# Kernel tuning notes

Hardware: AMD Instinct MI355X
Metric: run time of the kernel (lower is better)

Reference implementation:

```python
import jax, jax.numpy as jnp
import numpy as np

DIM = 384
DH = 32
H = DIM // DH          # 12 heads
N_WIN = 3072           # total windows
W_ACT = 1536           # active windows = M
T = 64                 # tokens per window (8x8)
NTOK = W_ACT * T       # 98304 active tokens
N_BLOCK = 9830
MLP = 4 * DIM
EPS = 1e-5


def _layer_norm(h, w, b):
    mu = jnp.mean(h, axis=-1, keepdims=True)
    var = jnp.mean(jnp.square(h - mu), axis=-1, keepdims=True)
    return (h - mu) * jax.lax.rsqrt(var + EPS) * w + b


def setup_inputs() -> dict:
    key = jax.random.key(0)
    ks = jax.random.split(key, 16)
    x = jax.random.normal(ks[0], (N_WIN, T, DIM), jnp.float32)
    # unique active windows, sorted (scatter-restore requires uniqueness)
    index_window = jnp.sort(jax.random.permutation(ks[1], N_WIN)[:W_ACT])
    # full permutation of active tokens into M groups of size S
    index_partition = jax.random.permutation(ks[2], NTOK)
    blocked_index = jax.random.permutation(ks[3], NTOK)[:N_BLOCK]
    s = 0.02
    params = dict(
        ln1_w=jnp.ones((DIM,), jnp.float32), ln1_b=jnp.zeros((DIM,), jnp.float32),
        qkv_w=jax.random.normal(ks[4], (3 * DIM, DIM), jnp.float32) * s,
        qkv_b=jnp.zeros((3 * DIM,), jnp.float32),
        proj_w=jax.random.normal(ks[5], (DIM, DIM), jnp.float32) * s,
        proj_b=jnp.zeros((DIM,), jnp.float32),
        ln2_w=jnp.ones((DIM,), jnp.float32), ln2_b=jnp.zeros((DIM,), jnp.float32),
        fc1_w=jax.random.normal(ks[6], (MLP, DIM), jnp.float32) * s,
        fc1_b=jnp.zeros((MLP,), jnp.float32),
        fc2_w=jax.random.normal(ks[7], (DIM, MLP), jnp.float32) * s,
        fc2_b=jnp.zeros((DIM,), jnp.float32),
    )
    return dict(x=x, index_window=index_window, index_partition=index_partition,
                blocked_index=blocked_index, M=W_ACT, K=jnp.zeros((1,), jnp.int64),
                **params)


def reference(x, index_window, index_partition, blocked_index, M, K,
              ln1_w, ln1_b, qkv_w, qkv_b, proj_w, proj_b,
              ln2_w, ln2_b, fc1_w, fc1_b, fc2_w, fc2_b):
    N, T_, C = x.shape
    scale = DH ** -0.5
    S = index_partition.shape[0] // M

    xn = _layer_norm(x, ln1_w, ln1_b)                      # (N, T, C)
    xw = xn[index_window].reshape(-1, C)                   # (NTOK, C) active tokens
    xp = xw[index_partition].reshape(M, S, C)              # (M, S, C) regrouped
    shortcut = xp

    qkv = (xp @ qkv_w.T + qkv_b).reshape(M, S, H, 3 * DH)  # per-head [q|k|v] chunks
    q, k, v = qkv[..., :DH], qkv[..., DH:2 * DH], qkv[..., 2 * DH:]

    attn = jnp.einsum('mqhd,mkhd->mhqk', q, k) * scale     # (M, H, Sq, Sk)

    # scatter scores into full-size map keyed by KEY token, mask blocked keys, gather back
    amap = jnp.zeros((xw.shape[0], S, H), attn.dtype)      # (NTOK, Sq, H)
    amap = amap.at[index_partition].set(jnp.transpose(attn, (0, 3, 2, 1)).reshape(-1, S, H))
    amap = amap.at[blocked_index].set(-10000.0)
    attn = jnp.transpose(amap[index_partition].reshape(M, S, S, H), (0, 3, 2, 1))
    attn = jax.nn.softmax(attn, axis=-1)

    o = jnp.einsum('mhqk,mkhd->mqhd', attn, v).reshape(M, S, C)
    o = o @ proj_w.T + proj_b

    # sub_layers: [Id, Id(+res), LN, fc1, GELU, fc2(+res)]
    h = shortcut + o
    shortcut = h
    h2 = _layer_norm(h, ln2_w, ln2_b)
    h2 = jax.nn.gelu(h2 @ fc1_w.T + fc1_b, approximate=False)
    h = shortcut + (h2 @ fc2_w.T + fc2_b)

    # scatter-restore: blocked tokens keep their (normed) input values
    XX = xw.at[index_partition].set(h.reshape(-1, C))
    XX = XX.at[blocked_index].set(xw[blocked_index])
    out = xn.at[index_window].set(XX.reshape(M, -1, C))
    return out
```

## Files before the change

### kernel.cpp

```cpp
#include <hip/hip_runtime.h>
#include <hip/hip_bf16.h>

typedef __attribute__((ext_vector_type(8))) short bf16x8;
typedef __attribute__((ext_vector_type(4))) short s16x4;
typedef __attribute__((ext_vector_type(4))) float f32x4;
typedef __attribute__((ext_vector_type(2))) long longx2;
typedef __attribute__((ext_vector_type(16))) unsigned char u8x16;

#define NW_   3072
#define WACT_ 1536
#define NTOK_ 98304
#define NBLK_ 9830
#define DIM_  384
#define QKVD_ 1152
#define MLPD_ 1536

__device__ __forceinline__ float bf2f(short s) {
  union { unsigned u; float f; } c;
  c.u = ((unsigned)(unsigned short)s) << 16;
  return c.f;
}
__device__ __forceinline__ short f2bf(float f) {
  union { float f; unsigned u; } c; c.f = f;
  unsigned lsb = (c.u >> 16) & 1u;
  c.u += 0x7fffu + lsb;
  return (short)(c.u >> 16);
}

__device__ __forceinline__ f32x4 mfma8(long a, long b, f32x4 c) {
  return __builtin_amdgcn_mfma_f32_16x16x32_fp8_fp8(a, b, c, 0, 0, 0);
}

__device__ __forceinline__ void gload16(const void* g, void* l) {
  __builtin_amdgcn_global_load_lds(
      (const __attribute__((address_space(1))) unsigned*)g,
      (__attribute__((address_space(3))) unsigned*)l, 16, 0, 0);
}

__device__ __forceinline__ int kperm(int col) {
  int l = (col >> 3) & 7;
  int s = ((l & 3) << 1) | (l >> 2);
  return (col & ~63) + s * 8 + (col & 7);
}

__device__ __forceinline__ void conv8_chunk(const float* __restrict__ src,
                                            unsigned char* __restrict__ dst,
                                            int K, int blk, int tid) {
  int i = (blk * 256 + tid) * 8;
  f32x4 v0 = *(const f32x4*)&src[i];
  f32x4 v1 = *(const f32x4*)&src[i + 4];
  int w0 = __builtin_amdgcn_cvt_pk_fp8_f32(v0[0], v0[1], 0, false);
  w0 = __builtin_amdgcn_cvt_pk_fp8_f32(v0[2], v0[3], w0, true);
  int w1 = __builtin_amdgcn_cvt_pk_fp8_f32(v1[0], v1[1], 0, false);
  w1 = __builtin_amdgcn_cvt_pk_fp8_f32(v1[2], v1[3], w1, true);
  int kro = i % K, row = i / K;
  union { int u[2]; long ll; } p; p.u[0] = w0; p.u[1] = w1;
  *(long*)&dst[(size_t)row * K + kperm(kro)] = p.ll;
}

__global__ __launch_bounds__(256) void pre_k(const float* __restrict__ qkvw,
                                             const float* __restrict__ projw,
                                             const float* __restrict__ fc1w,
                                             const float* __restrict__ fc2w,
                                             unsigned char* __restrict__ qw8,
                                             unsigned char* __restrict__ pw8,
                                             unsigned char* __restrict__ f1w8,
                                             unsigned char* __restrict__ f2w8,
                                             int* win_rank, unsigned* bitmap) {
  const int bid = blockIdx.x, tid = threadIdx.x;
  if (bid < 12) {
    int t = bid * 256 + tid;
    if (t < NW_) { win_rank[t] = -1; bitmap[t] = 0u; }
  } else if (bid < 228) {
    conv8_chunk(qkvw, qw8, 384, bid - 12, tid);
  } else if (bid < 300) {
    conv8_chunk(projw, pw8, 384, bid - 228, tid);
  } else if (bid < 588) {
    conv8_chunk(fc1w, f1w8, 384, bid - 300, tid);
  } else {
    conv8_chunk(fc2w, f2w8, MLPD_, bid - 588, tid);
  }
}

__global__ __launch_bounds__(256) void mapB_k(const int* __restrict__ iw,
                                              const int* __restrict__ blk,
                                              int* win_rank, unsigned* bitmap) {
  int t = blockIdx.x * 256 + threadIdx.x;
  if (t < WACT_) win_rank[iw[t]] = t;
  if (t < NBLK_) { int j = blk[t]; atomicOr(&bitmap[j >> 5], 1u << (j & 31)); }
}

__global__ __launch_bounds__(256) void mapC_k(const int* __restrict__ ip,
                                              const int* __restrict__ iw,
                                              const unsigned* __restrict__ bitmap,
                                              int* inv_ip, int* rowmap) {
  int i = blockIdx.x * 256 + threadIdx.x;
  if (i < NTOK_) {
    int j = ip[i];
    inv_ip[j] = i;
    int blocked = (bitmap[j >> 5] >> (j & 31)) & 1;
    rowmap[i] = blocked ? -1 : (iw[j >> 6] * 64 + (j & 63));
  }
}

__global__ __launch_bounds__(256) void ln1_k(const float* __restrict__ x,
                                             const float* __restrict__ w,
                                             const float* __restrict__ b,
                                             const int* __restrict__ win_rank,
                                             const int* __restrict__ inv_ip,
                                             const unsigned* __restrict__ bitmap,
                                             float* __restrict__ out,
                                             short* __restrict__ xp,
                                             unsigned char* __restrict__ xp8) {
  const int l = threadIdx.x & 31;
  const int tok = blockIdx.x * 8 + (threadIdx.x >> 5);
  const f32x4* xr = (const f32x4*)(x + (size_t)tok * DIM_);
  f32x4 v[3]; float s = 0.f;
#pragma unroll
  for (int j = 0; j < 3; ++j) {
    v[j] = xr[l + 32 * j];
    s += v[j][0] + v[j][1] + v[j][2] + v[j][3];
  }
#pragma unroll
  for (int m = 1; m <= 16; m <<= 1) s += __shfl_xor(s, m, 64);
  float mu = s * (1.0f / DIM_);
  float q = 0.f;
#pragma unroll
  for (int j = 0; j < 3; ++j)
#pragma unroll
    for (int e = 0; e < 4; ++e) { float d = v[j][e] - mu; q += d * d; }
#pragma unroll
  for (int m = 1; m <= 16; m <<= 1) q += __shfl_xor(q, m, 64);
  float rs = rsqrtf(q * (1.0f / DIM_) + 1e-5f);
  f32x4 y[3];
#pragma unroll
  for (int j = 0; j < 3; ++j) {
    f32x4 wv = *(const f32x4*)&w[4 * l + 128 * j];
    f32x4 bv = *(const f32x4*)&b[4 * l + 128 * j];
#pragma unroll
    for (int e = 0; e < 4; ++e) y[j][e] = (v[j][e] - mu) * rs * wv[e] + bv[e];
  }
  int wdw = tok >> 6, t = tok & 63;
  int rank = win_rank[wdw];
  if (rank < 0) {
    f32x4* po = (f32x4*)(out + (size_t)tok * DIM_);
#pragma unroll
    for (int j = 0; j < 3; ++j) po[l + 32 * j] = y[j];
  } else {
    int jdx = (rank << 6) + t;
    int i = inv_ip[jdx];
#pragma unroll
    for (int j = 0; j < 3; ++j) {
      s16x4 o;
#pragma unroll
      for (int e = 0; e < 4; ++e) o[e] = f2bf(y[j][e]);
      *(s16x4*)&xp[(size_t)i * DIM_ + 4 * l + 128 * j] = o;
      int wrd = __builtin_amdgcn_cvt_pk_fp8_f32(y[j][0], y[j][1], 0, false);
      wrd = __builtin_amdgcn_cvt_pk_fp8_f32(y[j][2], y[j][3], wrd, true);
      *(unsigned*)&xp8[(size_t)i * DIM_ + kperm(4 * l + 128 * j)] = (unsigned)wrd;
    }
    if ((bitmap[jdx >> 5] >> (jdx & 31)) & 1) {
      f32x4* po = (f32x4*)(out + (size_t)tok * DIM_);
#pragma unroll
      for (int j = 0; j < 3; ++j) po[l + 32 * j] = y[j];
    }
  }
}

__global__ __launch_bounds__(256) void ln2_k(const short* __restrict__ h,
                                             const float* __restrict__ w,
                                             const float* __restrict__ b,
                                             unsigned char* __restrict__ out8) {
  const int l = threadIdx.x & 31;
  const int tok = blockIdx.x * 8 + (threadIdx.x >> 5);
  const s16x4* xr = (const s16x4*)(h + (size_t)tok * DIM_);
  float v[12]; float s = 0.f;
#pragma unroll
  for (int j = 0; j < 3; ++j) {
    s16x4 rv = xr[l + 32 * j];
#pragma unroll
    for (int e = 0; e < 4; ++e) { v[j * 4 + e] = bf2f(rv[e]); s += v[j * 4 + e]; }
  }
#pragma unroll
  for (int m = 1; m <= 16; m <<= 1) s += __shfl_xor(s, m, 64);
  float mu = s * (1.0f / DIM_);
  float q = 0.f;
#pragma unroll
  for (int e = 0; e < 12; ++e) { float d = v[e] - mu; q += d * d; }
#pragma unroll
  for (int m = 1; m <= 16; m <<= 1) q += __shfl_xor(q, m, 64);
  float rs = rsqrtf(q * (1.0f / DIM_) + 1e-5f);
#pragma unroll
  for (int j = 0; j < 3; ++j) {
    f32x4 wv = *(const f32x4*)&w[4 * l + 128 * j];
    f32x4 bv = *(const f32x4*)&b[4 * l + 128 * j];
    float y[4];
#pragma unroll
    for (int e = 0; e < 4; ++e)
      y[e] = (v[j * 4 + e] - mu) * rs * wv[e] + bv[e];
    int wrd = __builtin_amdgcn_cvt_pk_fp8_f32(y[0], y[1], 0, false);
    wrd = __builtin_amdgcn_cvt_pk_fp8_f32(y[2], y[3], wrd, true);
    int c0 = 4 * l + 128 * j;
    *(unsigned*)&out8[(size_t)tok * DIM_ + kperm(c0)] = (unsigned)wrd;
  }
}

template <int EPI>
__global__ __launch_bounds__(512) void gemmf8_k(const unsigned char* __restrict__ A8,
                                                const unsigned char* __restrict__ B8,
                                                const float* __restrict__ bias,
                                                int K, int nx,
                                                short* __restrict__ Cb,
                                                unsigned char* __restrict__ C8,
                                                const short* __restrict__ add_bf,
                                                const int* __restrict__ rowmap,
                                                float* __restrict__ outf) {
  const int nwg = gridDim.x;
  const int q8 = nwg >> 3;
  const int wg = (blockIdx.x & 7) * q8 + (blockIdx.x >> 3);
  const int ntile = wg % nx, mtile = wg / nx;
  const int tid = threadIdx.x, wid = tid >> 6, lane = tid & 63;
  const int fq = lane >> 4, fr = lane & 15;
  const int wr = wid >> 1, wc = wid & 1;
  __shared__ __align__(16) unsigned char lA[256 * 128];
  __shared__ __align__(16) unsigned char lB[128 * 128];
  const int row0 = mtile * 256, col0 = ntile * 128;
  float bs[4];
#pragma unroll
  for (int nt = 0; nt < 4; ++nt) bs[nt] = bias[col0 + wc * 64 + nt * 16 + fr];
  f32x4 acc[4][4];
#pragma unroll
  for (int a = 0; a < 4; ++a)
#pragma unroll
    for (int c = 0; c < 4; ++c) acc[a][c] = (f32x4){0.f, 0.f, 0.f, 0.f};
  const int nkt = K >> 7;
  for (int kt = 0; kt < nkt; ++kt) {
    const int k0 = kt << 7;
#pragma unroll
    for (int i = 0; i < 4; ++i) {
      int g = i * 512 + tid;
      int r = g >> 3, c8 = g & 7;
      int s8 = c8 ^ (r & 7);
      gload16(A8 + (size_t)(row0 + r) * K + k0 + s8 * 16, (char*)lA + (size_t)g * 16);
    }
#pragma unroll
    for (int i = 0; i < 2; ++i) {
      int g = i * 512 + tid;
      int r = g >> 3, c8 = g & 7;
      int s8 = c8 ^ (r & 7);
      gload16(B8 + (size_t)(col0 + r) * K + k0 + s8 * 16, (char*)lB + (size_t)g * 16);
    }
    __syncthreads();
#pragma unroll
    for (int ss = 0; ss < 2; ++ss) {
      longx2 af[4], bfr[4];
      const int pb = ss * 4 + fq;
#pragma unroll
      for (int mt = 0; mt < 4; ++mt) {
        int r = wr * 64 + mt * 16 + fr;
        int d = pb ^ (r & 7);
        af[mt] = *(const longx2*)&lA[r * 128 + d * 16];
      }
#pragma unroll
      for (int nt = 0; nt < 4; ++nt) {
        int r = wc * 64 + nt * 16 + fr;
        int d = pb ^ (r & 7);
        bfr[nt] = *(const longx2*)&lB[r * 128 + d * 16];
      }
#pragma unroll
      for (int mt = 0; mt < 4; ++mt)
#pragma unroll
        for (int nt = 0; nt < 4; ++nt) {
          acc[mt][nt] = mfma8(af[mt][0], bfr[nt][0], acc[mt][nt]);
          acc[mt][nt] = mfma8(af[mt][1], bfr[nt][1], acc[mt][nt]);
        }
    }
    __syncthreads();
  }
#pragma unroll
  for (int mt = 0; mt < 4; ++mt) {
#pragma unroll
    for (int jj = 0; jj < 4; ++jj) {
      int r = row0 + wr * 64 + mt * 16 + fq * 4 + jj;
      int dmap = 0;
      if (EPI == 3) dmap = rowmap[r];
      if (EPI == 0) {
        float g4[4];
#pragma unroll
        for (int nt = 0; nt < 4; ++nt) g4[nt] = acc[mt][nt][jj] + bs[nt];
        int p01 = __builtin_amdgcn_cvt_pk_fp8_f32(g4[0], g4[1], 0, false);
        int p23 = __builtin_amdgcn_cvt_pk_fp8_f32(g4[2], g4[3], 0, false);
        const size_t rb = (size_t)r * QKVD_ + col0 + wc * 64 + fr;
        C8[rb]      = (unsigned char)(p01 & 0xff);
        C8[rb + 16] = (unsigned char)((p01 >> 8) & 0xff);
        C8[rb + 32] = (unsigned char)(p23 & 0xff);
        C8[rb + 48] = (unsigned char)((p23 >> 8) & 0xff);
      } else if (EPI == 1) {
#pragma unroll
        for (int nt = 0; nt < 4; ++nt) {
          int gcol = col0 + wc * 64 + nt * 16 + fr;
          float v = acc[mt][nt][jj] + bs[nt] + bf2f(add_bf[(size_t)r * DIM_ + gcol]);
          Cb[(size_t)r * DIM_ + gcol] = f2bf(v);
        }
      } else if (EPI == 2) {
        float g4[4];
#pragma unroll
        for (int nt = 0; nt < 4; ++nt) {
          float v = acc[mt][nt][jj] + bs[nt];
          float u = v * (0.79788456f + 0.03567741f * v * v);
          g4[nt] = v * __builtin_amdgcn_rcpf(1.0f + __expf(-2.0f * u));
        }
        int p01 = __builtin_amdgcn_cvt_pk_fp8_f32(g4[0], g4[1], 0, false);
        int p23 = __builtin_amdgcn_cvt_pk_fp8_f32(g4[2], g4[3], 0, false);
        const int C0 = col0 + wc * 64;
        const size_t rb = (size_t)r * MLPD_ + C0 + (fr & 7) + ((fr >> 3) << 4);
        C8[rb]      = (unsigned char)(p01 & 0xff);
        C8[rb + 32] = (unsigned char)((p01 >> 8) & 0xff);
        C8[rb + 8]  = (unsigned char)(p23 & 0xff);
        C8[rb + 40] = (unsigned char)((p23 >> 8) & 0xff);
      } else {
#pragma unroll
        for (int nt = 0; nt < 4; ++nt) {
          int gcol = col0 + wc * 64 + nt * 16 + fr;
          float v = acc[mt][nt][jj] + bs[nt] + bf2f(add_bf[(size_t)r * DIM_ + gcol]);
          if (dmap >= 0) outf[(size_t)dmap * DIM_ + gcol] = v;
        }
      }
    }
  }
}

__global__ __launch_bounds__(256) void attn_k(const unsigned char* __restrict__ qkv8,
                                              const unsigned* __restrict__ bitmap,
                                              const int* __restrict__ ip,
                                              unsigned char* __restrict__ o8) {
  const int flat = (blockIdx.x & 7) * 576 + (blockIdx.x >> 3);
  const int m = flat / 3;
  const int h = (flat % 3) * 4 + (threadIdx.x >> 6);
  const int wid = threadIdx.x >> 6, lane = threadIdx.x & 63;
  const int fq = lane >> 4, fr = lane & 15;
  __shared__ __align__(16) unsigned char P[4][64 * 72];
  __shared__ __align__(16) unsigned char Vt[4][32 * 72];
  __shared__ unsigned char flags[64];
  if (threadIdx.x < 64) {
    int j = ip[m * 64 + threadIdx.x];
    flags[threadIdx.x] = (unsigned char)((bitmap[j >> 5] >> (j & 31)) & 1);
  }
  __syncthreads();
  const float scale = 0.17677669529663687f;
  int msk[4];
#pragma unroll
  for (int nt = 0; nt < 4; ++nt) msk[nt] = flags[nt * 16 + fr];

  const unsigned char* base = qkv8 + (size_t)m * 64 * QKVD_ + h * 96;
  f32x4 sacc[4][4];
#pragma unroll
  for (int a = 0; a < 4; ++a)
#pragma unroll
    for (int c = 0; c < 4; ++c) sacc[a][c] = (f32x4){0.f, 0.f, 0.f, 0.f};
  long qa[4], kb[4];
#pragma unroll
  for (int mt = 0; mt < 4; ++mt)
    qa[mt] = *(const long*)(base + (size_t)(mt * 16 + fr) * QKVD_ + fq * 8);
#pragma unroll
  for (int nt = 0; nt < 4; ++nt)
    kb[nt] = *(const long*)(base + (size_t)(nt * 16 + fr) * QKVD_ + 32 + fq * 8);
#pragma unroll
  for (int mt = 0; mt < 4; ++mt)
#pragma unroll
    for (int nt = 0; nt < 4; ++nt)
      sacc[mt][nt] = mfma8(qa[mt], kb[nt], sacc[mt][nt]);
#pragma unroll
  for (int c = 0; c < 2; ++c) {
    u8x16 vv = *(const u8x16*)(base + (size_t)lane * QKVD_ + 64 + c * 16);
#pragma unroll
    for (int e = 0; e < 16; ++e) Vt[wid][(c * 16 + e) * 72 + lane] = vv[e];
  }
#pragma unroll
  for (int mt = 0; mt < 4; ++mt)
#pragma unroll
    for (int nt = 0; nt < 4; ++nt) {
      f32x4 sv = sacc[mt][nt];
#pragma unroll
      for (int jj = 0; jj < 4; ++jj)
        sv[jj] = msk[nt] ? -10000.0f : sv[jj] * scale;
      sacc[mt][nt] = sv;
    }
#pragma unroll
  for (int mt = 0; mt < 4; ++mt) {
#pragma unroll
    for (int jj = 0; jj < 4; ++jj) {
      float mx = sacc[mt][0][jj];
#pragma unroll
      for (int nt = 1; nt < 4; ++nt) mx = fmaxf(mx, sacc[mt][nt][jj]);
#pragma unroll
      for (int mm = 1; mm < 16; mm <<= 1) mx = fmaxf(mx, __shfl_xor(mx, mm, 64));
      float sm = 0.f;
      float p[4];
#pragma unroll
      for (int nt = 0; nt < 4; ++nt) {
        p[nt] = __expf(sacc[mt][nt][jj] - mx);
        sm += p[nt];
      }
#pragma unroll
      for (int mm = 1; mm < 16; mm <<= 1) sm += __shfl_xor(sm, mm, 64);
      float inv = 1.0f / sm;
      int rowb = (mt * 16 + fq * 4 + jj) * 72;
      int p01 = __builtin_amdgcn_cvt_pk_fp8_f32(p[0] * inv, p[1] * inv, 0, false);
      int p23 = __builtin_amdgcn_cvt_pk_fp8_f32(p[2] * inv, p[3] * inv, 0, false);
      P[wid][rowb + fr]      = (unsigned char)(p01 & 0xff);
      P[wid][rowb + 16 + fr] = (unsigned char)((p01 >> 8) & 0xff);
      P[wid][rowb + 32 + fr] = (unsigned char)(p23 & 0xff);
      P[wid][rowb + 48 + fr] = (unsigned char)((p23 >> 8) & 0xff);
    }
  }
  f32x4 oacc[4][2];
#pragma unroll
  for (int a = 0; a < 4; ++a)
#pragma unroll
    for (int c = 0; c < 2; ++c) oacc[a][c] = (f32x4){0.f, 0.f, 0.f, 0.f};
#pragma unroll
  for (int ks = 0; ks < 2; ++ks) {
    long pa[4], vb[2];
#pragma unroll
    for (int mt = 0; mt < 4; ++mt)
      pa[mt] = *(const long*)&P[wid][(mt * 16 + fr) * 72 + ks * 32 + fq * 8];
#pragma unroll
    for (int nd = 0; nd < 2; ++nd)
      vb[nd] = *(const long*)&Vt[wid][(nd * 16 + fr) * 72 + ks * 32 + fq * 8];
#pragma unroll
    for (int mt = 0; mt < 4; ++mt)
#pragma unroll
      for (int nd = 0; nd < 2; ++nd)
        oacc[mt][nd] = mfma8(pa[mt], vb[nd], oacc[mt][nd]);
  }
  const int pos0 = kperm(h * 32 + fr);
  const int pos1 = kperm(h * 32 + 16 + fr);
#pragma unroll
  for (int mt = 0; mt < 4; ++mt)
#pragma unroll
    for (int jj = 0; jj < 4; ++jj) {
      int p01 = __builtin_amdgcn_cvt_pk_fp8_f32(oacc[mt][0][jj], oacc[mt][1][jj],
                                                0, false);
      size_t rb = (size_t)(m * 64 + mt * 16 + fq * 4 + jj) * DIM_;
      o8[rb + pos0] = (unsigned char)(p01 & 0xff);
      o8[rb + pos1] = (unsigned char)((p01 >> 8) & 0xff);
    }
}

extern "C" void kernel_launch(void* const* d_in, const int* in_sizes, int n_in,
                              void* d_out, int out_size, void* d_ws, size_t ws_size,
                              hipStream_t stream) {
  const float* x = (const float*)d_in[0];
  const int* iw = (const int*)d_in[1];
  const int* ip = (const int*)d_in[2];
  const int* blk = (const int*)d_in[3];
  const float* ln1w = (const float*)d_in[6];
  const float* ln1b = (const float*)d_in[7];
  const float* qkvw = (const float*)d_in[8];
  const float* qkvb = (const float*)d_in[9];
  const float* projw = (const float*)d_in[10];
  const float* projb = (const float*)d_in[11];
  const float* ln2w = (const float*)d_in[12];
  const float* ln2b = (const float*)d_in[13];
  const float* fc1w = (const float*)d_in[14];
  const float* fc1b = (const float*)d_in[15];
  const float* fc2w = (const float*)d_in[16];
  const float* fc2b = (const float*)d_in[17];
  float* out = (float*)d_out;

  char* ws = (char*)d_ws;
  unsigned char* qkvw8 = (unsigned char*)ws;
  unsigned char* projw8 = (unsigned char*)(ws + 442368);
  unsigned char* fc1w8 = (unsigned char*)(ws + 589824);
  unsigned char* fc2w8 = (unsigned char*)(ws + 1179648);
  int* inv_ip = (int*)(ws + 2211840);
  int* rowmap = inv_ip + NTOK_;
  int* win_rank = rowmap + NTOK_;
  unsigned* bitmap = (unsigned*)(win_rank + NW_);
  short* xp = (short*)(ws + 4349952);
  unsigned char* qkv8 = (unsigned char*)(ws + 79847424);
  unsigned char* t8 = qkv8;
  unsigned char* obuf8 = (unsigned char*)(ws + 306339840);
  unsigned char* ln2buf8 = (unsigned char*)(ws + 344088576);
  unsigned char* xp8 = (unsigned char*)(ws + 381837312);
  short* hbuf = (short*)(ws + 457334784);
  (void)in_sizes; (void)n_in; (void)out_size; (void)ws_size;

  pre_k<<<876, 256, 0, stream>>>(qkvw, projw, fc1w, fc2w, qkvw8, projw8, fc1w8,
                                 fc2w8, win_rank, bitmap);
  mapB_k<<<39, 256, 0, stream>>>(iw, blk, win_rank, bitmap);
  mapC_k<<<NTOK_ / 256, 256, 0, stream>>>(ip, iw, bitmap, inv_ip, rowmap);
  ln1_k<<<(NW_ * 64) / 8, 256, 0, stream>>>(x, ln1w, ln1b, win_rank, inv_ip, bitmap,
                                            out, xp, xp8);
  gemmf8_k<0><<<384 * 9, 512, 0, stream>>>(xp8, qkvw8, qkvb, 384, 9, nullptr,
                                           qkv8, nullptr, nullptr, nullptr);
  attn_k<<<WACT_ * 3, 256, 0, stream>>>(qkv8, bitmap, ip, obuf8);
  gemmf8_k<1><<<384 * 3, 512, 0, stream>>>(obuf8, projw8, projb, 384, 3, hbuf,
                                           nullptr, xp, nullptr, nullptr);
  ln2_k<<<NTOK_ / 8, 256, 0, stream>>>(hbuf, ln2w, ln2b, ln2buf8);
  gemmf8_k<2><<<384 * 12, 512, 0, stream>>>(ln2buf8, fc1w8, fc1b, 384, 12, nullptr,
                                            t8, nullptr, nullptr, nullptr);
  gemmf8_k<3><<<384 * 3, 512, 0, stream>>>(t8, fc2w8, fc2b, MLPD_, 3, nullptr,
                                           nullptr, hbuf, rowmap, out);
}
```

Baseline: 609.7 us.

## Stage window QKV rows into swizzled LDS with coalesced loads in attention kernel

Measured after the change: 609.4 us (median of 2 runs). No clear change (-0.1%).

```diff
diff --git a/kernel.cpp b/kernel.cpp
--- a/kernel.cpp
+++ b/kernel.cpp
@@ -5,7 +5,6 @@
 typedef __attribute__((ext_vector_type(4))) short s16x4;
 typedef __attribute__((ext_vector_type(4))) float f32x4;
 typedef __attribute__((ext_vector_type(2))) long longx2;
-typedef __attribute__((ext_vector_type(16))) unsigned char u8x16;
 
 #define NW_   3072
 #define WACT_ 1536
@@ -336,23 +335,39 @@
                                               unsigned char* __restrict__ o8) {
   const int flat = (blockIdx.x & 7) * 576 + (blockIdx.x >> 3);
   const int m = flat / 3;
-  const int h = (flat % 3) * 4 + (threadIdx.x >> 6);
+  const int grp = flat % 3;
   const int wid = threadIdx.x >> 6, lane = threadIdx.x & 63;
+  const int h = grp * 4 + wid;
   const int fq = lane >> 4, fr = lane & 15;
-  __shared__ __align__(16) unsigned char P[4][64 * 72];
+  __shared__ __align__(16) unsigned char qkvL[24576];
   __shared__ __align__(16) unsigned char Vt[4][32 * 72];
   __shared__ unsigned char flags[64];
+  unsigned char (*P)[64 * 72] = (unsigned char (*)[64 * 72])qkvL;
+
+  const unsigned char* rowbase = qkv8 + (size_t)m * 64 * QKVD_ + grp * 384;
+#pragma unroll
+  for (int i = 0; i < 6; ++i) {
+    int g = i * 256 + threadIdx.x;
+    int r = g / 24, c16 = g % 24;
+    int sc = c16 ^ (r & 7);
+    gload16(rowbase + (size_t)r * QKVD_ + sc * 16, (char*)qkvL + (size_t)g * 16);
+  }
   if (threadIdx.x < 64) {
     int j = ip[m * 64 + threadIdx.x];
     flags[threadIdx.x] = (unsigned char)((bitmap[j >> 5] >> (j & 31)) & 1);
   }
   __syncthreads();
+
   const float scale = 0.17677669529663687f;
   int msk[4];
 #pragma unroll
   for (int nt = 0; nt < 4; ++nt) msk[nt] = flags[nt * 16 + fr];
 
-  const unsigned char* base = qkv8 + (size_t)m * 64 * QKVD_ + h * 96;
+  auto ldsc = [&](int r, int c) -> long {
+    int slot = (c >> 1) ^ (r & 7);
+    return *(const long*)&qkvL[r * 384 + slot * 16 + (c & 1) * 8];
+  };
+
   f32x4 sacc[4][4];
 #pragma unroll
   for (int a = 0; a < 4; ++a)
@@ -360,22 +375,23 @@
     for (int c = 0; c < 4; ++c) sacc[a][c] = (f32x4){0.f, 0.f, 0.f, 0.f};
   long qa[4], kb[4];
 #pragma unroll
-  for (int mt = 0; mt < 4; ++mt)
-    qa[mt] = *(const long*)(base + (size_t)(mt * 16 + fr) * QKVD_ + fq * 8);
-#pragma unroll
-  for (int nt = 0; nt < 4; ++nt)
-    kb[nt] = *(const long*)(base + (size_t)(nt * 16 + fr) * QKVD_ + 32 + fq * 8);
+  for (int mt = 0; mt < 4; ++mt) qa[mt] = ldsc(mt * 16 + fr, wid * 12 + fq);
+#pragma unroll
+  for (int nt = 0; nt < 4; ++nt) kb[nt] = ldsc(nt * 16 + fr, wid * 12 + 4 + fq);
 #pragma unroll
   for (int mt = 0; mt < 4; ++mt)
 #pragma unroll
     for (int nt = 0; nt < 4; ++nt)
       sacc[mt][nt] = mfma8(qa[mt], kb[nt], sacc[mt][nt]);
 #pragma unroll
-  for (int c = 0; c < 2; ++c) {
-    u8x16 vv = *(const u8x16*)(base + (size_t)lane * QKVD_ + 64 + c * 16);
-#pragma unroll
-    for (int e = 0; e < 16; ++e) Vt[wid][(c * 16 + e) * 72 + lane] = vv[e];
-  }
+  for (int cc = 0; cc < 4; ++cc) {
+    long vv = ldsc(lane, wid * 12 + 8 + cc);
+    const unsigned char* vb = (const unsigned char*)&vv;
+#pragma unroll
+    for (int e = 0; e < 8; ++e) Vt[wid][(cc * 8 + e) * 72 + lane] = vb[e];
+  }
+  __syncthreads();
+
 #pragma unroll
   for (int mt = 0; mt < 4; ++mt)
 #pragma unroll
```
